# Performance work log

Measured on AMD Instinct MI355X. Metric: run time of the kernel, lower is better.

Reference implementation:

```python
import jax, jax.numpy as jnp
import numpy as np

MASK_VALUE = -1000000.0


def setup_inputs() -> dict:
    key = jax.random.key(0)
    k1, k2, k3, k4 = jax.random.split(key, 4)
    B, Lq, Lk, d = 32, 1024, 1024, 128
    return {
        "query": jax.random.normal(k1, (B, Lq, d), dtype=jnp.float32),
        "key": jax.random.normal(k2, (B, Lk, d), dtype=jnp.float32),
        "value": jax.random.normal(k3, (B, Lk, d), dtype=jnp.float32),
        "valid_length": jax.random.randint(k4, (B,), 0, Lk, dtype=jnp.int64),
    }


def reference(query, key, value, valid_length):
    # query [B, Lq, d], key/value [B, Lk, d], valid_length [B]
    d = query.shape[-1]
    # scores [B, Lq, Lk]
    scores = jnp.einsum("bqd,bkd->bqk", query, key) / jnp.sqrt(jnp.float32(d))
    Lk = key.shape[1]
    # mask positions >= valid_length with -1e6 (per-batch, broadcast over Lq)
    pos = jnp.arange(Lk)  # [Lk]
    mask = pos[None, None, :] >= valid_length[:, None, None]  # [B, 1, Lk]
    scores = jnp.where(mask, MASK_VALUE, scores)
    attn = jax.nn.softmax(scores, axis=-1)
    # dropout p=0.0 in eval -> identity
    return jnp.einsum("bqk,bkd->bqd", attn, value)
```

## Files before the change

### kernel.cpp

```cpp
#include <hip/hip_runtime.h>

#define B_N 32
#define LQ  1024
#define LK  1024
#define DH  128

typedef __attribute__((ext_vector_type(4))) float    f32x4;
typedef __attribute__((ext_vector_type(8))) short    s16x8;
typedef __attribute__((ext_vector_type(4))) _Float16 f16x4;
typedef __attribute__((ext_vector_type(8))) _Float16 f16x8;

__device__ inline unsigned short f2bf(float f) {
    union { float f; unsigned u; } c; c.f = f;
    unsigned u = c.u;
    u += 0x7fffu + ((u >> 16) & 1u);
    return (unsigned short)(u >> 16);
}

#define ESCALE 0.12751743f

#define G2L16(gp, lp) __builtin_amdgcn_global_load_lds(                         \
    (const __attribute__((address_space(1))) void*)(gp),                        \
    (__attribute__((address_space(3))) void*)(lp), 16, 0, 0)

__global__ __launch_bounds__(256)
void prep_kv(const float* __restrict__ K, const float* __restrict__ V,
             const int* __restrict__ VL,
             unsigned short* __restrict__ Kb, _Float16* __restrict__ Vt)
{
    __shared__ float tl[32 * 132];
    const int tid  = threadIdx.x;
    const int lane = tid & 63;
    const int wv   = tid >> 6;
    const int n    = lane & 15;
    const int quad = lane >> 4;

    const int  idx = blockIdx.x;
    const bool isK = (idx >> 10) == 0;
    const int  b   = (idx & 7) | (((idx >> 3) & 3) << 3);
    const int  kt  = (idx >> 5) & 31;

    const int vl = VL[b];
    if (isK) {
        if (vl <= 0 || kt >= 2 * ((vl + 63) >> 6)) return;
    } else {
        const int nch = (vl > 0) ? ((vl + 63) >> 6) : 16;
        if (kt >= 2 * nch) return;
    }

    const float4* src = (const float4*)((isK ? K : V) + ((size_t)b * LK + kt * 32) * DH);
    #pragma unroll
    for (int h = 0; h < 4; ++h) {
        const int i2 = h * 256 + tid;
        const int row = i2 >> 5, c4 = i2 & 31;
        *(float4*)&tl[row * 132 + c4 * 4] = src[i2];
    }
    __syncthreads();

    if (isK) {
        union { s16x8 v; unsigned short u[8]; } t8;
        #pragma unroll
        for (int h = 0; h < 2; ++h) {
            const int f = wv * 2 + h;
            const int tt2 = f >> 2, s = f & 3;
            const float* p = &tl[(tt2 * 16 + n) * 132 + s * 32 + quad * 8];
            const float4 a = *(const float4*)p;
            const float4 c = *(const float4*)(p + 4);
            t8.u[0] = f2bf(a.x); t8.u[1] = f2bf(a.y); t8.u[2] = f2bf(a.z); t8.u[3] = f2bf(a.w);
            t8.u[4] = f2bf(c.x); t8.u[5] = f2bf(c.y); t8.u[6] = f2bf(c.z); t8.u[7] = f2bf(c.w);
            const int w = b * 256 + (kt * 2 + tt2) * 4 + s;
            *(s16x8*)(Kb + (size_t)w * 512 + lane * 8) = t8.v;
        }
    } else {
        #pragma unroll
        for (int h = 0; h < 2; ++h) {
            const int f  = wv * 2 + h;
            const int kg = f >> 2, dp = f & 3;
            f16x8 t8;
            #pragma unroll
            for (int i = 0; i < 4; ++i) {
                const float* row = &tl[(kg * 16 + quad * 4 + i) * 132 + dp * 32 + n];
                t8[i]     = (_Float16)row[0];
                t8[4 + i] = (_Float16)row[16];
            }
            const int v = (b * 64 + kt * 2 + kg) * 4 + dp;
            *(f16x8*)(Vt + (size_t)v * 512 + lane * 8) = t8;
        }
    }
}

__global__ __launch_bounds__(256)
void attn_fwd(const float* __restrict__ Q, const unsigned short* __restrict__ Kb,
              const _Float16* __restrict__ Vt, const int* __restrict__ VL,
              float* __restrict__ O)
{
    __shared__ __align__(16) unsigned short bufK[2][16 * 512];
    __shared__ __align__(16) _Float16       bufV[2][16 * 512];

    const int tid  = threadIdx.x;
    const int lane = tid & 63;
    const int w    = tid >> 6;
    const int quad = lane >> 4;
    const int m16  = lane & 15;

    const int idx = blockIdx.x;
    const int qg  = (idx >> 5) & 15;
    const int b   = (idx & 7) | ((((idx >> 3) + (idx >> 8)) & 3) << 3);
    const int q0  = qg * 64;

    const int vl  = VL[b];
    const int nch = (vl > 0) ? ((vl + 63) >> 6) : 16;
    const float emaskval = (vl == 0) ? 1.0f : 0.0f;

    s16x8 qf[4];
    {
        const float* qrow = Q + ((size_t)b * LQ + q0 + w * 16 + m16) * DH + quad * 8;
        #pragma unroll
        for (int s = 0; s < 4; ++s) {
            const float4 a = *(const float4*)(qrow + s * 32);
            const float4 c = *(const float4*)(qrow + s * 32 + 4);
            union { s16x8 v; unsigned short u[8]; } t;
            t.u[0] = f2bf(a.x); t.u[1] = f2bf(a.y); t.u[2] = f2bf(a.z); t.u[3] = f2bf(a.w);
            t.u[4] = f2bf(c.x); t.u[5] = f2bf(c.y); t.u[6] = f2bf(c.z); t.u[7] = f2bf(c.w);
            qf[s] = t.v;
        }
    }

    f32x4 o[8];
    #pragma unroll
    for (int dt = 0; dt < 8; ++dt) o[dt] = (f32x4){0.f, 0.f, 0.f, 0.f};
    float lrun = 0.f;

    const unsigned short* kg0 = Kb + (size_t)b * (256 * 512);
    const _Float16*       vg0 = Vt + (size_t)b * (256 * 512);
    const int co = tid * 8;

#define STAGE(c, t)                                                             \
    do {                                                                        \
        const unsigned short* gk_ = kg0 + (size_t)(t) * 8192;                   \
        const _Float16*       gv_ = vg0 + (size_t)(t) * 8192;                   \
        _Pragma("unroll")                                                       \
        for (int it_ = 0; it_ < 4; ++it_)                                       \
            G2L16(gk_ + it_ * 2048 + co, &bufK[c][it_ * 2048 + co]);            \
        _Pragma("unroll")                                                       \
        for (int it_ = 0; it_ < 4; ++it_)                                       \
            G2L16(gv_ + it_ * 2048 + co, &bufV[c][it_ * 2048 + co]);            \
    } while (0)

    STAGE(0, 0);
    asm volatile("s_waitcnt vmcnt(0)" ::: "memory");
    __builtin_amdgcn_sched_barrier(0);
    __builtin_amdgcn_s_barrier();

    int cur = 0;
    for (int t = 0; t < nch; ++t) {
        if (t + 1 < nch) STAGE(cur ^ 1, t + 1);

        const unsigned short* bk = &bufK[cur][0];
        const _Float16*       bv = &bufV[cur][0];
        const bool maskc = (t * 64 + 64 > vl);
        f16x4 pA[4];

        #pragma unroll
        for (int g = 0; g < 4; ++g) {
            f32x4 st = (f32x4){0.f, 0.f, 0.f, 0.f};
            #pragma unroll
            for (int s = 0; s < 4; ++s) {
                const s16x8 kf = *(const s16x8*)(bk + (g * 4 + s) * 512 + lane * 8);
                st = __builtin_amdgcn_mfma_f32_16x16x32_bf16(kf, qf[s], st, 0, 0, 0);
            }
            #pragma unroll
            for (int i = 0; i < 4; ++i) {
                float e = __builtin_amdgcn_exp2f(st[i] * ESCALE);
                if (maskc && (t * 64 + g * 16 + quad * 4 + i >= vl)) e = emaskval;
                lrun += e;
                pA[g][i] = (_Float16)e;
            }
        }

        #pragma unroll
        for (int g = 0; g < 4; ++g) {
            #pragma unroll
            for (int dp = 0; dp < 4; ++dp) {
                const f16x8 w8 = *(const f16x8*)(bv + (g * 4 + dp) * 512 + lane * 8);
                const f16x4 lo = __builtin_shufflevector(w8, w8, 0, 1, 2, 3);
                const f16x4 hi = __builtin_shufflevector(w8, w8, 4, 5, 6, 7);
                o[dp * 2]     = __builtin_amdgcn_mfma_f32_16x16x16f16(pA[g], lo, o[dp * 2],     0, 0, 0);
                o[dp * 2 + 1] = __builtin_amdgcn_mfma_f32_16x16x16f16(pA[g], hi, o[dp * 2 + 1], 0, 0, 0);
            }
        }

        asm volatile("s_waitcnt vmcnt(0)" ::: "memory");
        __builtin_amdgcn_sched_barrier(0);
        __builtin_amdgcn_s_barrier();
        cur ^= 1;
    }
#undef STAGE

    float L = lrun;
    L += __shfl_xor(L, 16);
    L += __shfl_xor(L, 32);
    const size_t obase = ((size_t)b * LQ + q0 + w * 16 + quad * 4) * DH + m16;
    #pragma unroll
    for (int r = 0; r < 4; ++r) {
        const float inv = 1.0f / __shfl(L, quad * 4 + r);
        #pragma unroll
        for (int dt = 0; dt < 8; ++dt)
            O[obase + (size_t)r * DH + dt * 16] = o[dt][r] * inv;
    }
}

extern "C" void kernel_launch(void* const* d_in, const int* in_sizes, int n_in,
                              void* d_out, int out_size, void* d_ws, size_t ws_size,
                              hipStream_t stream) {
    const float* Q  = (const float*)d_in[0];
    const float* K  = (const float*)d_in[1];
    const float* V  = (const float*)d_in[2];
    const int*   VL = (const int*)d_in[3];
    float* O = (float*)d_out;
    (void)in_sizes; (void)n_in; (void)out_size; (void)ws_size;

    unsigned short* Kb = (unsigned short*)d_ws;
    _Float16*       Vt = (_Float16*)(Kb + (size_t)B_N * 256 * 512);

    prep_kv<<<dim3(2048), dim3(256), 0, stream>>>(K, V, VL, Kb, Vt);
    attn_fwd<<<dim3(B_N * (LQ / 64)), dim3(256), 0, stream>>>(Q, Kb, Vt, VL, O);
}
```

Before: 115.3 us.

## Give each wave two 16-row query tiles and halve the attention block to 128 threads

Each wave now handles 32 query rows as two 16-row sub-tiles, so each K and V fragment read from LDS feeds two MFMAs. The block shrinks to two waves while still covering 64 query rows, and the global-to-LDS staging loop issues twice as many loads per thread. This cuts LDS read traffic per unit of MFMA work. In exchange it doubles accumulator and Q-fragment registers per thread and leaves fewer waves per block to hide latency.

```diff
diff --git a/kernel.cpp b/kernel.cpp
--- a/kernel.cpp
+++ b/kernel.cpp
@@ -89,7 +89,7 @@
     }
 }
 
-__global__ __launch_bounds__(256)
+__global__ __launch_bounds__(128)
 void attn_fwd(const float* __restrict__ Q, const unsigned short* __restrict__ Kb,
               const _Float16* __restrict__ Vt, const int* __restrict__ VL,
               float* __restrict__ O)
@@ -112,9 +112,10 @@
     const int nch = (vl > 0) ? ((vl + 63) >> 6) : 16;
     const float emaskval = (vl == 0) ? 1.0f : 0.0f;
 
-    s16x8 qf[4];
-    {
-        const float* qrow = Q + ((size_t)b * LQ + q0 + w * 16 + m16) * DH + quad * 8;
+    s16x8 qf[2][4];
+    #pragma unroll
+    for (int h = 0; h < 2; ++h) {
+        const float* qrow = Q + ((size_t)b * LQ + q0 + w * 32 + h * 16 + m16) * DH + quad * 8;
         #pragma unroll
         for (int s = 0; s < 4; ++s) {
             const float4 a = *(const float4*)(qrow + s * 32);
@@ -122,14 +123,16 @@
             union { s16x8 v; unsigned short u[8]; } t;
             t.u[0] = f2bf(a.x); t.u[1] = f2bf(a.y); t.u[2] = f2bf(a.z); t.u[3] = f2bf(a.w);
             t.u[4] = f2bf(c.x); t.u[5] = f2bf(c.y); t.u[6] = f2bf(c.z); t.u[7] = f2bf(c.w);
-            qf[s] = t.v;
-        }
-    }
-
-    f32x4 o[8];
-    #pragma unroll
-    for (int dt = 0; dt < 8; ++dt) o[dt] = (f32x4){0.f, 0.f, 0.f, 0.f};
-    float lrun = 0.f;
+            qf[h][s] = t.v;
+        }
+    }
+
+    f32x4 o[2][8];
+    #pragma unroll
+    for (int h = 0; h < 2; ++h)
+        #pragma unroll
+        for (int dt = 0; dt < 8; ++dt) o[h][dt] = (f32x4){0.f, 0.f, 0.f, 0.f};
+    float lrun[2] = {0.f, 0.f};
 
     const unsigned short* kg0 = Kb + (size_t)b * (256 * 512);
     const _Float16*       vg0 = Vt + (size_t)b * (256 * 512);
@@ -140,11 +143,11 @@
         const unsigned short* gk_ = kg0 + (size_t)(t) * 8192;                   \
         const _Float16*       gv_ = vg0 + (size_t)(t) * 8192;                   \
         _Pragma("unroll")                                                       \
-        for (int it_ = 0; it_ < 4; ++it_)                                       \
-            G2L16(gk_ + it_ * 2048 + co, &bufK[c][it_ * 2048 + co]);            \
+        for (int it_ = 0; it_ < 8; ++it_)                                       \
+            G2L16(gk_ + it_ * 1024 + co, &bufK[c][it_ * 1024 + co]);            \
         _Pragma("unroll")                                                       \
-        for (int it_ = 0; it_ < 4; ++it_)                                       \
-            G2L16(gv_ + it_ * 2048 + co, &bufV[c][it_ * 2048 + co]);            \
+        for (int it_ = 0; it_ < 8; ++it_)                                       \
+            G2L16(gv_ + it_ * 1024 + co, &bufV[c][it_ * 1024 + co]);            \
     } while (0)
 
     STAGE(0, 0);
@@ -159,22 +162,26 @@
         const unsigned short* bk = &bufK[cur][0];
         const _Float16*       bv = &bufV[cur][0];
         const bool maskc = (t * 64 + 64 > vl);
-        f16x4 pA[4];
+        f16x4 pA[2][4];
 
         #pragma unroll
         for (int g = 0; g < 4; ++g) {
-            f32x4 st = (f32x4){0.f, 0.f, 0.f, 0.f};
+            f32x4 st0 = (f32x4){0.f, 0.f, 0.f, 0.f};
+            f32x4 st1 = (f32x4){0.f, 0.f, 0.f, 0.f};
             #pragma unroll
             for (int s = 0; s < 4; ++s) {
                 const s16x8 kf = *(const s16x8*)(bk + (g * 4 + s) * 512 + lane * 8);
-                st = __builtin_amdgcn_mfma_f32_16x16x32_bf16(kf, qf[s], st, 0, 0, 0);
+                st0 = __builtin_amdgcn_mfma_f32_16x16x32_bf16(kf, qf[0][s], st0, 0, 0, 0);
+                st1 = __builtin_amdgcn_mfma_f32_16x16x32_bf16(kf, qf[1][s], st1, 0, 0, 0);
             }
             #pragma unroll
             for (int i = 0; i < 4; ++i) {
-                float e = __builtin_amdgcn_exp2f(st[i] * ESCALE);
-                if (maskc && (t * 64 + g * 16 + quad * 4 + i >= vl)) e = emaskval;
-                lrun += e;
-                pA[g][i] = (_Float16)e;
+                float e0 = __builtin_amdgcn_exp2f(st0[i] * ESCALE);
+                float e1 = __builtin_amdgcn_exp2f(st1[i] * ESCALE);
+                if (maskc && (t * 64 + g * 16 + quad * 4 + i >= vl)) { e0 = emaskval; e1 = emaskval; }
+                lrun[0] += e0; lrun[1] += e1;
+                pA[0][g][i] = (_Float16)e0;
+                pA[1][g][i] = (_Float16)e1;
             }
         }
 
@@ -185,8 +192,10 @@
                 const f16x8 w8 = *(const f16x8*)(bv + (g * 4 + dp) * 512 + lane * 8);
                 const f16x4 lo = __builtin_shufflevector(w8, w8, 0, 1, 2, 3);
                 const f16x4 hi = __builtin_shufflevector(w8, w8, 4, 5, 6, 7);
-                o[dp * 2]     = __builtin_amdgcn_mfma_f32_16x16x16f16(pA[g], lo, o[dp * 2],     0, 0, 0);
-                o[dp * 2 + 1] = __builtin_amdgcn_mfma_f32_16x16x16f16(pA[g], hi, o[dp * 2 + 1], 0, 0, 0);
+                o[0][dp * 2]     = __builtin_amdgcn_mfma_f32_16x16x16f16(pA[0][g], lo, o[0][dp * 2],     0, 0, 0);
+                o[0][dp * 2 + 1] = __builtin_amdgcn_mfma_f32_16x16x16f16(pA[0][g], hi, o[0][dp * 2 + 1], 0, 0, 0);
+                o[1][dp * 2]     = __builtin_amdgcn_mfma_f32_16x16x16f16(pA[1][g], lo, o[1][dp * 2],     0, 0, 0);
+                o[1][dp * 2 + 1] = __builtin_amdgcn_mfma_f32_16x16x16f16(pA[1][g], hi, o[1][dp * 2 + 1], 0, 0, 0);
             }
         }
 
@@ -197,16 +206,19 @@
     }
 #undef STAGE
 
-    float L = lrun;
-    L += __shfl_xor(L, 16);
-    L += __shfl_xor(L, 32);
-    const size_t obase = ((size_t)b * LQ + q0 + w * 16 + quad * 4) * DH + m16;
-    #pragma unroll
-    for (int r = 0; r < 4; ++r) {
-        const float inv = 1.0f / __shfl(L, quad * 4 + r);
-        #pragma unroll
-        for (int dt = 0; dt < 8; ++dt)
-            O[obase + (size_t)r * DH + dt * 16] = o[dt][r] * inv;
+    #pragma unroll
+    for (int h = 0; h < 2; ++h) {
+        float L = lrun[h];
+        L += __shfl_xor(L, 16);
+        L += __shfl_xor(L, 32);
+        const size_t obase = ((size_t)b * LQ + q0 + w * 32 + h * 16 + quad * 4) * DH + m16;
+        #pragma unroll
+        for (int r = 0; r < 4; ++r) {
+            const float inv = 1.0f / __shfl(L, quad * 4 + r);
+            #pragma unroll
+            for (int dt = 0; dt < 8; ++dt)
+                O[obase + (size_t)r * DH + dt * 16] = o[h][dt][r] * inv;
+        }
     }
 }
 
@@ -224,5 +236,5 @@
     _Float16*       Vt = (_Float16*)(Kb + (size_t)B_N * 256 * 512);
 
     prep_kv<<<dim3(2048), dim3(256), 0, stream>>>(K, V, VL, Kb, Vt);
-    attn_fwd<<<dim3(B_N * (LQ / 64)), dim3(256), 0, stream>>>(Q, Kb, Vt, VL, O);
-}
+    attn_fwd<<<dim3(B_N * (LQ / 64)), dim3(128), 0, stream>>>(Q, Kb, Vt, VL, O);
+}
```

New measurement: 121.6 us. 1.05x slower.
